# Optimization experiments

Measured on AMD Instinct MI355X. Metric: run time of the kernel, lower is better.

The kernel has to match this reference:

```python
import jax, jax.numpy as jnp
import numpy as np

# Static module config (matches init_kwargs; note forward requires P == Np)
Np = 60   # particles
P  = 60   # per-particle features
Nv = 14   # secondary vertices
S  = 5    # per-vertex features
De = 20
Do = 24
HID = 60
NPP = Np * (Np - 1)
NPV = Np * Nv

# Edge list replacing the dense one-hot Rr/Rs matmuls.
# Edges are all ordered pairs (i, j), i != j, ordered by receiver i then sender j,
# so edges with the same receiver are contiguous (enables reshape+sum scatter).
_pairs = np.array([(i, j) for i in range(Np) for j in range(Np) if i != j], dtype=np.int64)
RECV = jnp.asarray(_pairs[:, 0])  # [NPP]
SEND = jnp.asarray(_pairs[:, 1])  # [NPP]


def _mlp(h, W1, b1, W2, b2):
    return jax.nn.relu(h @ W1 + b1) @ W2 + b2


def setup_inputs() -> dict:
    key = jax.random.key(0)
    ks = jax.random.split(key, 9)
    B = 1024

    def lin(k, fi, fo):
        kw, kb = jax.random.split(k)
        s = 1.0 / np.sqrt(fi)
        W = jax.random.uniform(kw, (fi, fo), minval=-s, maxval=s, dtype=jnp.float32)
        b = jax.random.uniform(kb, (fo,), minval=-s, maxval=s, dtype=jnp.float32)
        return W, b

    W1_pp, b1_pp = lin(ks[0], 2 * P, HID)
    W2_pp, b2_pp = lin(ks[1], HID, De)
    W1_pv, b1_pv = lin(ks[2], P + S, HID)
    W2_pv, b2_pv = lin(ks[3], HID, De)
    W1_o, b1_o = lin(ks[4], P + De, HID)
    W2_o, b2_o = lin(ks[5], HID, Do)
    Wc, bc = lin(ks[6], Do, 1)
    x = jax.random.normal(ks[7], (B, P, Np), dtype=jnp.float32)
    y = jax.random.normal(ks[8], (B, S, Nv), dtype=jnp.float32)
    return dict(x=x, y=y,
                W1_pp=W1_pp, b1_pp=b1_pp, W2_pp=W2_pp, b2_pp=b2_pp,
                W1_pv=W1_pv, b1_pv=b1_pv, W2_pv=W2_pv, b2_pv=b2_pv,
                W1_o=W1_o, b1_o=b1_o, W2_o=W2_o, b2_o=b2_o,
                Wc=Wc, bc=bc)


def reference(x, y, W1_pp, b1_pp, W2_pp, b2_pp, W1_pv, b1_pv, W2_pv, b2_pv,
              W1_o, b1_o, W2_o, b2_o, Wc, bc):
    Bb = x.shape[0]
    # particle-particle branch: gather (x @ Rr, x @ Rs) as index takes
    Orr = jnp.take(x, RECV, axis=2)                  # [B, P, NPP]
    Ors = jnp.take(x, SEND, axis=2)                  # [B, P, NPP]
    Bcat = jnp.concatenate([Orr, Ors], axis=1)       # [B, 2P, NPP]
    # Faithful to the original: B.view(-1, 2P) WITHOUT transposing (row-major flatten)
    E = _mlp(Bcat.reshape(-1, 2 * P), W1_pp, b1_pp, W2_pp, b2_pp).reshape(Bb, NPP, De)
    E = jnp.swapaxes(E, 1, 2)                        # [B, De, NPP]
    # scatter-sum E @ Rr.T : edges grouped by receiver -> reshape+sum
    Ebar_pp = E.reshape(Bb, De, Np, Np - 1).sum(axis=-1)   # [B, De, Np]
    # particle-vertex branch: t = i*Nv + v
    Ork = jnp.repeat(x, Nv, axis=2)                  # [B, P, NPV]  (x @ Rk)
    Orv = jnp.tile(y, (1, 1, Np))                    # [B, S, NPV]  (y @ Rv)
    C = jnp.swapaxes(jnp.concatenate([Ork, Orv], axis=1), 1, 2)  # [B, NPV, P+S]
    F = _mlp(C.reshape(-1, P + S), W1_pv, b1_pv, W2_pv, b2_pv).reshape(Bb, NPV, De)
    F = jnp.swapaxes(F, 1, 2)                        # [B, De, NPV]
    Ebar_pv = F.reshape(Bb, De, Np, Nv).sum(axis=-1)  # F @ Rk.T  -> [B, De, Np]
    Ebar = jnp.swapaxes(Ebar_pp + Ebar_pv, 1, 2)     # [B, Np, De]
    J = jnp.concatenate([x, Ebar], axis=2)           # [B, Np, P+De] (requires P==Np)
    O = _mlp(J.reshape(-1, P + De), W1_o, b1_o, W2_o, b2_o).reshape(Bb, Np, Do)
    O = O.sum(axis=1)                                # transpose+sum over particles -> [B, Do]
    O = O @ Wc + bc                                  # [B, 1]
    return jax.nn.sigmoid(O)
```

## Files before the change

kernel.cpp:

```cpp
#include <hip/hip_runtime.h>
#include <hip/hip_bf16.h>
#include <math.h>

typedef __attribute__((ext_vector_type(8))) short short8;
typedef __attribute__((ext_vector_type(4))) float f32x4;

namespace {
constexpr int XP = 61;
constexpr int EB0 = 3660;
constexpr int Y0 = 4860;
constexpr int ZSLOT = 4930;
constexpr int ARENA_W = 4931;

constexpr int NTAB_PP = 222 * 4 * 64 * 8;
constexpr int NTAB_PV = 53 * 3 * 64 * 8;
constexpr int NTAB_O  = 4 * 3 * 64 * 8;
constexpr int TABPP_B = 0;
constexpr int TABPV_B = TABPP_B + NTAB_PP * 2;
constexpr int TABO_B  = TABPV_B + NTAB_PV * 2;
constexpr int WPP1_B  = TABO_B + NTAB_O * 2;
constexpr int WPP2_B  = WPP1_B + 16 * 64 * 16;
constexpr int WPV1_B  = WPP2_B + 4 * 64 * 16;
constexpr int WPV2_B  = WPV1_B + 12 * 64 * 16;
constexpr int WO1_B   = WPV2_B + 4 * 64 * 16;
constexpr int WO2_B   = WO1_B + 12 * 64 * 16;
constexpr int BIAS_B  = WO2_B + 4 * 64 * 16;
}

__device__ __forceinline__ short f2bfs(float f) {
  __hip_bfloat16 h = __float2bfloat16(f);
  short s;
  __builtin_memcpy(&s, &h, 2);
  return s;
}

__global__ __launch_bounds__(256) void build_tables(char* wsb) {
  int t = blockIdx.x * 256 + threadIdx.x;
  unsigned short* tpp = (unsigned short*)(wsb + TABPP_B);
  unsigned short* tpv = (unsigned short*)(wsb + TABPV_B);
  unsigned short* tou = (unsigned short*)(wsb + TABO_B);
  if (t < NTAB_PP) {
    int j = t & 7, l = (t >> 3) & 63, blk = t >> 9;
    int ks = blk & 3, mt = blk >> 2;
    int rr = mt * 16 + (l & 15), k = ks * 32 + (l >> 4) * 8 + j;
    unsigned off = ZSLOT;
    if (rr < 3540 && k < 120) {
      unsigned p = (unsigned)rr * 120u + (unsigned)k;
      unsigned f = p / 3540u, e = p - f * 3540u;
      unsigned i = e / 59u, jj = e - i * 59u;
      unsigned col = (f < 60u) ? i : ((jj < i) ? jj : jj + 1u);
      unsigned ft = (f < 60u) ? f : f - 60u;
      off = ft * (unsigned)XP + col;
    }
    tpp[t] = (unsigned short)(off * 4u);
    return;
  }
  t -= NTAB_PP;
  if (t < NTAB_PV) {
    int j = t & 7, l = (t >> 3) & 63, blk = t >> 9;
    int ks = blk % 3, mt = blk / 3;
    int tt = mt * 16 + (l & 15), k = ks * 32 + (l >> 4) * 8 + j;
    unsigned off = ZSLOT;
    if (tt < 840 && k < 65) {
      int i = tt / 14, v = tt - i * 14;
      off = (k < 60) ? (unsigned)(k * XP + i) : (unsigned)(Y0 + (k - 60) * 14 + v);
    }
    tpv[t] = (unsigned short)(off * 4u);
    return;
  }
  t -= NTAB_PV;
  if (t < NTAB_O) {
    int j = t & 7, l = (t >> 3) & 63, blk = t >> 9;
    int ks = blk % 3, mt = blk / 3;
    int r = mt * 16 + (l & 15), k = ks * 32 + (l >> 4) * 8 + j;
    unsigned off = ZSLOT;
    if (r < 60 && k < 80)
      off = (k < 60) ? (unsigned)(r * XP + k) : (unsigned)(EB0 + r * 20 + (k - 60));
    tou[t] = (unsigned short)(off * 4u);
  }
}

__global__ __launch_bounds__(256) void build_wfrag(char* wsb,
    const float* W1pp, const float* W2pp, const float* W1pv, const float* W2pv,
    const float* W1o, const float* W2o,
    const float* b1pp, const float* b2pp, const float* b1pv, const float* b2pv,
    const float* b1o, const float* b2o) {
  int t = blockIdx.x * 256 + threadIdx.x;
  if (t < 13312) {
    const float* W; int Kt, Nt, NTt; unsigned* dst; int local;
    if (t < 4096)       { W = W1pp; Kt = 120; Nt = 60; NTt = 4; dst = (unsigned*)(wsb + WPP1_B); local = t; }
    else if (t < 5120)  { W = W2pp; Kt = 60;  Nt = 20; NTt = 2; dst = (unsigned*)(wsb + WPP2_B); local = t - 4096; }
    else if (t < 8192)  { W = W1pv; Kt = 65;  Nt = 60; NTt = 4; dst = (unsigned*)(wsb + WPV1_B); local = t - 5120; }
    else if (t < 9216)  { W = W2pv; Kt = 60;  Nt = 20; NTt = 2; dst = (unsigned*)(wsb + WPV2_B); local = t - 8192; }
    else if (t < 12288) { W = W1o;  Kt = 80;  Nt = 60; NTt = 4; dst = (unsigned*)(wsb + WO1_B);  local = t - 9216; }
    else                { W = W2o;  Kt = 60;  Nt = 24; NTt = 2; dst = (unsigned*)(wsb + WO2_B);  local = t - 12288; }
    int d = local & 3, l = (local >> 2) & 63, rest = local >> 8;
    int nt = rest % NTt, ks = rest / NTt;
    int k = ks * 32 + (l >> 4) * 8 + 2 * d, n = nt * 16 + (l & 15);
    float v0 = (k < Kt && n < Nt) ? W[k * Nt + n] : 0.f;
    float v1 = (k + 1 < Kt && n < Nt) ? W[(k + 1) * Nt + n] : 0.f;
    unsigned u0 = (unsigned short)f2bfs(v0);
    unsigned u1 = (unsigned short)f2bfs(v1);
    dst[local] = u0 | (u1 << 16);
    return;
  }
  t -= 13312;
  if (t < 288) {
    float* bd = (float*)(wsb + BIAS_B);
    float v = 0.f;
    if (t < 64)       { if (t < 60) v = b1pp[t]; }
    else if (t < 96)  { int n = t - 64;  if (n < 20) v = b2pp[n]; }
    else if (t < 160) { int n = t - 96;  if (n < 60) v = b1pv[n]; }
    else if (t < 192) { int n = t - 160; if (n < 20) v = b2pv[n]; }
    else if (t < 256) { int n = t - 192; if (n < 60) v = b1o[n]; }
    else              { int n = t - 256; if (n < 24) v = b2o[n]; }
    bd[t] = v;
  }
}

__device__ __forceinline__ short8 gather8(const char* xb, uint4 tw) {
  float g0 = *(const float*)(xb + (tw.x & 0xffffu));
  float g1 = *(const float*)(xb + (tw.x >> 16));
  float g2 = *(const float*)(xb + (tw.y & 0xffffu));
  float g3 = *(const float*)(xb + (tw.y >> 16));
  float g4 = *(const float*)(xb + (tw.z & 0xffffu));
  float g5 = *(const float*)(xb + (tw.z >> 16));
  float g6 = *(const float*)(xb + (tw.w & 0xffffu));
  float g7 = *(const float*)(xb + (tw.w >> 16));
  short8 af;
  af[0] = f2bfs(g0); af[1] = f2bfs(g1); af[2] = f2bfs(g2); af[3] = f2bfs(g3);
  af[4] = f2bfs(g4); af[5] = f2bfs(g5); af[6] = f2bfs(g6); af[7] = f2bfs(g7);
  return af;
}

template <int NKS>
__device__ __forceinline__ void mlp_tile(
    int mt, int lane, const uint4* __restrict__ tab,
    const short8* wf1, const short8* wf2,
    const float (&b1v)[4], const float (&b2v)[2],
    const float* arena, short (*hrow)[72], f32x4 (&a2)[2])
{
  const int cl = lane & 15, qq = lane >> 4;
  const char* xb = (const char*)arena;

  f32x4 acc[4];
#pragma unroll
  for (int nt = 0; nt < 4; ++nt) {
    float bv = b1v[nt];
    acc[nt] = (f32x4){bv, bv, bv, bv};
  }

#pragma unroll
  for (int ks = 0; ks < NKS; ++ks) {
    uint4 tw = tab[(mt * NKS + ks) * 64 + lane];
    short8 af = gather8(xb, tw);
#pragma unroll
    for (int nt = 0; nt < 4; ++nt) {
      short8 wf = wf1[(ks * 4 + nt) * 64 + lane];
      acc[nt] = __builtin_amdgcn_mfma_f32_16x16x32_bf16(af, wf, acc[nt], 0, 0, 0);
    }
  }

#pragma unroll
  for (int nt = 0; nt < 4; ++nt)
#pragma unroll
    for (int r = 0; r < 4; ++r)
      hrow[qq * 4 + r][nt * 16 + cl] = f2bfs(fmaxf(acc[nt][r], 0.f));

#pragma unroll
  for (int nt = 0; nt < 2; ++nt) {
    float bv = b2v[nt];
    a2[nt] = (f32x4){bv, bv, bv, bv};
  }
#pragma unroll
  for (int k2 = 0; k2 < 2; ++k2) {
    short8 h = *(const short8*)&hrow[cl][k2 * 32 + qq * 8];
#pragma unroll
    for (int nt = 0; nt < 2; ++nt) {
      short8 wf = wf2[(k2 * 2 + nt) * 64 + lane];
      a2[nt] = __builtin_amdgcn_mfma_f32_16x16x32_bf16(h, wf, a2[nt], 0, 0, 0);
    }
  }
}

template <int DIV, int LIM>
__device__ __forceinline__ void scatter_e(const f32x4 (&a2)[2], int rb, float* eb, int cl) {
  int riA = rb / DIV, riB = (rb + 3) / DIV;
#pragma unroll
  for (int nt = 0; nt < 2; ++nt) {
    int col = nt * 16 + cl;
    if (col < 20) {
      if (riA == riB && rb + 3 < LIM) {
        atomicAdd(&eb[riA * 20 + col], a2[nt][0] + a2[nt][1] + a2[nt][2] + a2[nt][3]);
      } else {
#pragma unroll
        for (int r = 0; r < 4; ++r) {
          int rr = rb + r;
          if (rr < LIM) atomicAdd(&eb[(rr / DIV) * 20 + col], a2[nt][r]);
        }
      }
    }
  }
}

__global__ __launch_bounds__(256, 3) void fused_kernel(
    const float* __restrict__ x, const float* __restrict__ y,
    const float* __restrict__ Wc, const float* __restrict__ Bc,
    const char* __restrict__ wsb, float* __restrict__ out) {
  __shared__ float arena[ARENA_W];
  __shared__ __align__(16) short wlds[20 * 64 * 8];
  __shared__ short hlds[4][16][72];
  __shared__ float osum[24];

  const int b = blockIdx.x;
  const int tid = threadIdx.x;
  const int w = tid >> 6;
  const int lane = tid & 63;
  const int cl = lane & 15, q4 = (lane >> 4) * 4;

  for (int k = tid; k < 3600; k += 256) {
    int r = k / 60, c = k - r * 60;
    arena[r * XP + c] = x[(size_t)b * 3600 + k];
  }
  if (tid < 70) arena[Y0 + tid] = y[(size_t)b * 70 + tid];
  for (int k = tid; k < 1200; k += 256) arena[EB0 + k] = 0.f;
  if (tid == 0) arena[ZSLOT] = 0.f;
  if (tid < 24) osum[tid] = 0.f;
  {
    uint4* d = (uint4*)wlds;
    const uint4* sgl = (const uint4*)(wsb + WPP1_B);
    for (int k = tid; k < 1280; k += 256) d[k] = sgl[k];
  }
  __syncthreads();

  const float* biasf = (const float*)(wsb + BIAS_B);

  {
    const short8* wf1 = (const short8*)wlds;
    const short8* wf2 = (const short8*)wlds + 16 * 64;
    const uint4* tab = (const uint4*)(wsb + TABPP_B);
    float b1v[4], b2v[2];
#pragma unroll
    for (int nt = 0; nt < 4; ++nt) b1v[nt] = biasf[0 + nt * 16 + cl];
#pragma unroll
    for (int nt = 0; nt < 2; ++nt) b2v[nt] = biasf[64 + nt * 16 + cl];

    for (int mt = w; mt < 222; mt += 4) {
      f32x4 a2[2];
      mlp_tile<4>(mt, lane, tab, wf1, wf2, b1v, b2v, arena, hlds[w], a2);
      scatter_e<59, 3540>(a2, mt * 16 + q4, &arena[EB0], cl);
    }
  }

  __syncthreads();
  {
    uint4* d = (uint4*)wlds;
    const uint4* sgl = (const uint4*)(wsb + WPV1_B);
    for (int k = tid; k < 1024; k += 256) d[k] = sgl[k];
  }
  __syncthreads();

  {
    const short8* wf1 = (const short8*)wlds;
    const short8* wf2 = (const short8*)wlds + 12 * 64;
    const uint4* tab = (const uint4*)(wsb + TABPV_B);
    float b1v[4], b2v[2];
#pragma unroll
    for (int nt = 0; nt < 4; ++nt) b1v[nt] = biasf[96 + nt * 16 + cl];
#pragma unroll
    for (int nt = 0; nt < 2; ++nt) b2v[nt] = biasf[160 + nt * 16 + cl];

    for (int mt = w; mt < 53; mt += 4) {
      f32x4 a2[2];
      mlp_tile<3>(mt, lane, tab, wf1, wf2, b1v, b2v, arena, hlds[w], a2);
      scatter_e<14, 840>(a2, mt * 16 + q4, &arena[EB0], cl);
    }
  }

  __syncthreads();
  {
    uint4* d = (uint4*)wlds;
    const uint4* sgl = (const uint4*)(wsb + WO1_B);
    for (int k = tid; k < 1024; k += 256) d[k] = sgl[k];
  }
  __syncthreads();

  {
    const short8* wf1 = (const short8*)wlds;
    const short8* wf2 = (const short8*)wlds + 12 * 64;
    const uint4* tab = (const uint4*)(wsb + TABO_B);
    float b1v[4], b2v[2];
#pragma unroll
    for (int nt = 0; nt < 4; ++nt) b1v[nt] = biasf[192 + nt * 16 + cl];
#pragma unroll
    for (int nt = 0; nt < 2; ++nt) b2v[nt] = biasf[256 + nt * 16 + cl];

    f32x4 a2[2];
    mlp_tile<3>(w, lane, tab, wf1, wf2, b1v, b2v, arena, hlds[w], a2);
    int rb = w * 16 + q4;
#pragma unroll
    for (int nt = 0; nt < 2; ++nt) {
      int col = nt * 16 + cl;
      if (col < 24) {
        if (rb + 3 < 60) {
          atomicAdd(&osum[col], a2[nt][0] + a2[nt][1] + a2[nt][2] + a2[nt][3]);
        } else {
#pragma unroll
          for (int r = 0; r < 4; ++r)
            if (rb + r < 60) atomicAdd(&osum[col], a2[nt][r]);
        }
      }
    }
  }

  __syncthreads();
  if (tid == 0) {
    float sd = Bc[0];
#pragma unroll
    for (int o = 0; o < 24; ++o) sd = fmaf(osum[o], Wc[o], sd);
    out[b] = 1.f / (1.f + expf(-sd));
  }
}

extern "C" void kernel_launch(void* const* d_in, const int* in_sizes, int n_in,
                              void* d_out, int out_size, void* d_ws, size_t ws_size,
                              hipStream_t stream) {
  const float* x     = (const float*)d_in[0];
  const float* y     = (const float*)d_in[1];
  const float* W1_pp = (const float*)d_in[2];
  const float* b1_pp = (const float*)d_in[3];
  const float* W2_pp = (const float*)d_in[4];
  const float* b2_pp = (const float*)d_in[5];
  const float* W1_pv = (const float*)d_in[6];
  const float* b1_pv = (const float*)d_in[7];
  const float* W2_pv = (const float*)d_in[8];
  const float* b2_pv = (const float*)d_in[9];
  const float* W1_o  = (const float*)d_in[10];
  const float* b1_o  = (const float*)d_in[11];
  const float* W2_o  = (const float*)d_in[12];
  const float* b2_o  = (const float*)d_in[13];
  const float* Wc    = (const float*)d_in[14];
  const float* bc    = (const float*)d_in[15];
  float* out = (float*)d_out;
  char* wsb = (char*)d_ws;

  const int Bb = in_sizes[0] / 3600;
  const int tab_total = NTAB_PP + NTAB_PV + NTAB_O;

  build_tables<<<(tab_total + 255) / 256, 256, 0, stream>>>(wsb);
  build_wfrag<<<(13600 + 255) / 256, 256, 0, stream>>>(wsb,
      W1_pp, W2_pp, W1_pv, W2_pv, W1_o, W2_o,
      b1_pp, b2_pp, b1_pv, b2_pv, b1_o, b2_o);
  fused_kernel<<<Bb, 256, 0, stream>>>(x, y, Wc, bc, wsb, out);
}
```

Measured before the change: 336.8 us.

## Switch MLP tiles to 32x32x16 MFMA and store activations as bf16 in LDS

Replaces the 16x16x32 bf16 MFMA tiling with 32x32x16 tiles, so each wave handles 32 edge rows per tile with two N-tiles for the hidden layer and one for the output layer. The gather tables, weight fragments and edge-aggregation scatter are re-laid-out to match. The per-block x/y arena and the aggregated edge features are converted to bf16 once at load time, so each gather is a 16-bit LDS read with no per-element conversion. The aim is fewer MFMA issues, fewer table and weight loads, and less conversion work. In exchange the padding waste changes, the output stage uses only two waves, and accumulator register pressure per wave rises.

```diff
diff --git a/kernel.cpp b/kernel.cpp
--- a/kernel.cpp
+++ b/kernel.cpp
@@ -3,34 +3,42 @@
 #include <math.h>
 
 typedef __attribute__((ext_vector_type(8))) short short8;
-typedef __attribute__((ext_vector_type(4))) float f32x4;
+typedef __attribute__((ext_vector_type(16))) float f32x16;
 
 namespace {
-constexpr int XP = 61;
-constexpr int EB0 = 3660;
-constexpr int Y0 = 4860;
-constexpr int ZSLOT = 4930;
-constexpr int ARENA_W = 4931;
-
-constexpr int NTAB_PP = 222 * 4 * 64 * 8;
-constexpr int NTAB_PV = 53 * 3 * 64 * 8;
-constexpr int NTAB_O  = 4 * 3 * 64 * 8;
+constexpr int XB0 = 0;
+constexpr int EBF0 = 7440;
+constexpr int EBB0 = 12240;
+constexpr int YB0 = 14640;
+constexpr int ZS = 14780;
+constexpr int ARENA_B = 14784;
+
+constexpr int NTAB_PP = 111 * 8 * 64 * 8;
+constexpr int NTAB_PV = 27 * 5 * 64 * 8;
+constexpr int NTAB_O  = 2 * 5 * 64 * 8;
 constexpr int TABPP_B = 0;
 constexpr int TABPV_B = TABPP_B + NTAB_PP * 2;
 constexpr int TABO_B  = TABPV_B + NTAB_PV * 2;
 constexpr int WPP1_B  = TABO_B + NTAB_O * 2;
-constexpr int WPP2_B  = WPP1_B + 16 * 64 * 16;
-constexpr int WPV1_B  = WPP2_B + 4 * 64 * 16;
-constexpr int WPV2_B  = WPV1_B + 12 * 64 * 16;
-constexpr int WO1_B   = WPV2_B + 4 * 64 * 16;
-constexpr int WO2_B   = WO1_B + 12 * 64 * 16;
-constexpr int BIAS_B  = WO2_B + 4 * 64 * 16;
+constexpr int WPP2_B  = WPP1_B + 16 * 1024;
+constexpr int WPV1_B  = WPP2_B + 4 * 1024;
+constexpr int WPV2_B  = WPV1_B + 10 * 1024;
+constexpr int WO1_B   = WPV2_B + 4 * 1024;
+constexpr int WO2_B   = WO1_B + 10 * 1024;
+constexpr int BIAS_B  = WO2_B + 4 * 1024;
 }
 
 __device__ __forceinline__ short f2bfs(float f) {
   __hip_bfloat16 h = __float2bfloat16(f);
   short s;
   __builtin_memcpy(&s, &h, 2);
+  return s;
+}
+
+__device__ __forceinline__ f32x16 splat16(float v) {
+  f32x16 s;
+#pragma unroll
+  for (int i = 0; i < 16; ++i) s[i] = v;
   return s;
 }
 
@@ -41,42 +49,44 @@
   unsigned short* tou = (unsigned short*)(wsb + TABO_B);
   if (t < NTAB_PP) {
     int j = t & 7, l = (t >> 3) & 63, blk = t >> 9;
-    int ks = blk & 3, mt = blk >> 2;
-    int rr = mt * 16 + (l & 15), k = ks * 32 + (l >> 4) * 8 + j;
-    unsigned off = ZSLOT;
+    int ks = blk & 7, mt = blk >> 3;
+    int rr = mt * 32 + (l & 31), k = ks * 16 + ((l >> 5) * 8) + j;
+    unsigned off = ZS;
     if (rr < 3540 && k < 120) {
       unsigned p = (unsigned)rr * 120u + (unsigned)k;
       unsigned f = p / 3540u, e = p - f * 3540u;
       unsigned i = e / 59u, jj = e - i * 59u;
       unsigned col = (f < 60u) ? i : ((jj < i) ? jj : jj + 1u);
       unsigned ft = (f < 60u) ? f : f - 60u;
-      off = ft * (unsigned)XP + col;
-    }
-    tpp[t] = (unsigned short)(off * 4u);
+      off = XB0 + (ft * 62u + col) * 2u;
+    }
+    tpp[t] = (unsigned short)off;
     return;
   }
   t -= NTAB_PP;
   if (t < NTAB_PV) {
     int j = t & 7, l = (t >> 3) & 63, blk = t >> 9;
-    int ks = blk % 3, mt = blk / 3;
-    int tt = mt * 16 + (l & 15), k = ks * 32 + (l >> 4) * 8 + j;
-    unsigned off = ZSLOT;
+    int ks = blk % 5, mt = blk / 5;
+    int tt = mt * 32 + (l & 31), k = ks * 16 + ((l >> 5) * 8) + j;
+    unsigned off = ZS;
     if (tt < 840 && k < 65) {
       int i = tt / 14, v = tt - i * 14;
-      off = (k < 60) ? (unsigned)(k * XP + i) : (unsigned)(Y0 + (k - 60) * 14 + v);
-    }
-    tpv[t] = (unsigned short)(off * 4u);
+      off = (k < 60) ? (unsigned)(XB0 + (k * 62 + i) * 2)
+                     : (unsigned)(YB0 + ((k - 60) * 14 + v) * 2);
+    }
+    tpv[t] = (unsigned short)off;
     return;
   }
   t -= NTAB_PV;
   if (t < NTAB_O) {
     int j = t & 7, l = (t >> 3) & 63, blk = t >> 9;
-    int ks = blk % 3, mt = blk / 3;
-    int r = mt * 16 + (l & 15), k = ks * 32 + (l >> 4) * 8 + j;
-    unsigned off = ZSLOT;
+    int ks = blk % 5, mt = blk / 5;
+    int r = mt * 32 + (l & 31), k = ks * 16 + ((l >> 5) * 8) + j;
+    unsigned off = ZS;
     if (r < 60 && k < 80)
-      off = (k < 60) ? (unsigned)(r * XP + k) : (unsigned)(EB0 + r * 20 + (k - 60));
-    tou[t] = (unsigned short)(off * 4u);
+      off = (k < 60) ? (unsigned)(XB0 + (r * 62 + k) * 2)
+                     : (unsigned)(EBB0 + (r * 20 + (k - 60)) * 2);
+    tou[t] = (unsigned short)off;
   }
 }
 
@@ -86,17 +96,17 @@
     const float* b1pp, const float* b2pp, const float* b1pv, const float* b2pv,
     const float* b1o, const float* b2o) {
   int t = blockIdx.x * 256 + threadIdx.x;
-  if (t < 13312) {
-    const float* W; int Kt, Nt, NTt; unsigned* dst; int local;
-    if (t < 4096)       { W = W1pp; Kt = 120; Nt = 60; NTt = 4; dst = (unsigned*)(wsb + WPP1_B); local = t; }
-    else if (t < 5120)  { W = W2pp; Kt = 60;  Nt = 20; NTt = 2; dst = (unsigned*)(wsb + WPP2_B); local = t - 4096; }
-    else if (t < 8192)  { W = W1pv; Kt = 65;  Nt = 60; NTt = 4; dst = (unsigned*)(wsb + WPV1_B); local = t - 5120; }
-    else if (t < 9216)  { W = W2pv; Kt = 60;  Nt = 20; NTt = 2; dst = (unsigned*)(wsb + WPV2_B); local = t - 8192; }
-    else if (t < 12288) { W = W1o;  Kt = 80;  Nt = 60; NTt = 4; dst = (unsigned*)(wsb + WO1_B);  local = t - 9216; }
-    else                { W = W2o;  Kt = 60;  Nt = 24; NTt = 2; dst = (unsigned*)(wsb + WO2_B);  local = t - 12288; }
-    int d = local & 3, l = (local >> 2) & 63, rest = local >> 8;
-    int nt = rest % NTt, ks = rest / NTt;
-    int k = ks * 32 + (l >> 4) * 8 + 2 * d, n = nt * 16 + (l & 15);
+  if (t < 12288) {
+    const float* W; int Kt, Nt, NT; unsigned* dst; int local;
+    if (t < 4096)        { W = W1pp; Kt = 120; Nt = 60; NT = 2; dst = (unsigned*)(wsb + WPP1_B); local = t; }
+    else if (t < 5120)   { W = W2pp; Kt = 60;  Nt = 20; NT = 1; dst = (unsigned*)(wsb + WPP2_B); local = t - 4096; }
+    else if (t < 7680)   { W = W1pv; Kt = 65;  Nt = 60; NT = 2; dst = (unsigned*)(wsb + WPV1_B); local = t - 5120; }
+    else if (t < 8704)   { W = W2pv; Kt = 60;  Nt = 20; NT = 1; dst = (unsigned*)(wsb + WPV2_B); local = t - 7680; }
+    else if (t < 11264)  { W = W1o;  Kt = 80;  Nt = 60; NT = 2; dst = (unsigned*)(wsb + WO1_B);  local = t - 8704; }
+    else                 { W = W2o;  Kt = 60;  Nt = 24; NT = 1; dst = (unsigned*)(wsb + WO2_B);  local = t - 11264; }
+    int d = local & 3, l = (local >> 2) & 63, fi = local >> 8;
+    int nt = fi % NT, ks = fi / NT;
+    int k = ks * 16 + (l >> 5) * 8 + 2 * d, n = nt * 32 + (l & 31);
     float v0 = (k < Kt && n < Nt) ? W[k * Nt + n] : 0.f;
     float v1 = (k + 1 < Kt && n < Nt) ? W[(k + 1) * Nt + n] : 0.f;
     unsigned u0 = (unsigned short)f2bfs(v0);
@@ -104,7 +114,7 @@
     dst[local] = u0 | (u1 << 16);
     return;
   }
-  t -= 13312;
+  t -= 12288;
   if (t < 288) {
     float* bd = (float*)(wsb + BIAS_B);
     float v = 0.f;
@@ -118,85 +128,70 @@
   }
 }
 
-__device__ __forceinline__ short8 gather8(const char* xb, uint4 tw) {
-  float g0 = *(const float*)(xb + (tw.x & 0xffffu));
-  float g1 = *(const float*)(xb + (tw.x >> 16));
-  float g2 = *(const float*)(xb + (tw.y & 0xffffu));
-  float g3 = *(const float*)(xb + (tw.y >> 16));
-  float g4 = *(const float*)(xb + (tw.z & 0xffffu));
-  float g5 = *(const float*)(xb + (tw.z >> 16));
-  float g6 = *(const float*)(xb + (tw.w & 0xffffu));
-  float g7 = *(const float*)(xb + (tw.w >> 16));
-  short8 af;
-  af[0] = f2bfs(g0); af[1] = f2bfs(g1); af[2] = f2bfs(g2); af[3] = f2bfs(g3);
-  af[4] = f2bfs(g4); af[5] = f2bfs(g5); af[6] = f2bfs(g6); af[7] = f2bfs(g7);
-  return af;
-}
-
 template <int NKS>
-__device__ __forceinline__ void mlp_tile(
+__device__ __forceinline__ void mlp32(
     int mt, int lane, const uint4* __restrict__ tab,
     const short8* wf1, const short8* wf2,
-    const float (&b1v)[4], const float (&b2v)[2],
-    const float* arena, short (*hrow)[72], f32x4 (&a2)[2])
+    float b1a, float b1b, float b2,
+    const unsigned char* arena_b, short (*hrow)[72], f32x16& eo)
 {
-  const int cl = lane & 15, qq = lane >> 4;
-  const char* xb = (const char*)arena;
-
-  f32x4 acc[4];
-#pragma unroll
-  for (int nt = 0; nt < 4; ++nt) {
-    float bv = b1v[nt];
-    acc[nt] = (f32x4){bv, bv, bv, bv};
-  }
+  const int cl = lane & 31, hi = lane >> 5;
+
+  f32x16 acc0 = splat16(b1a);
+  f32x16 acc1 = splat16(b1b);
 
 #pragma unroll
   for (int ks = 0; ks < NKS; ++ks) {
     uint4 tw = tab[(mt * NKS + ks) * 64 + lane];
-    short8 af = gather8(xb, tw);
-#pragma unroll
-    for (int nt = 0; nt < 4; ++nt) {
-      short8 wf = wf1[(ks * 4 + nt) * 64 + lane];
-      acc[nt] = __builtin_amdgcn_mfma_f32_16x16x32_bf16(af, wf, acc[nt], 0, 0, 0);
-    }
-  }
-
-#pragma unroll
-  for (int nt = 0; nt < 4; ++nt)
-#pragma unroll
-    for (int r = 0; r < 4; ++r)
-      hrow[qq * 4 + r][nt * 16 + cl] = f2bfs(fmaxf(acc[nt][r], 0.f));
-
-#pragma unroll
-  for (int nt = 0; nt < 2; ++nt) {
-    float bv = b2v[nt];
-    a2[nt] = (f32x4){bv, bv, bv, bv};
-  }
-#pragma unroll
-  for (int k2 = 0; k2 < 2; ++k2) {
-    short8 h = *(const short8*)&hrow[cl][k2 * 32 + qq * 8];
-#pragma unroll
-    for (int nt = 0; nt < 2; ++nt) {
-      short8 wf = wf2[(k2 * 2 + nt) * 64 + lane];
-      a2[nt] = __builtin_amdgcn_mfma_f32_16x16x32_bf16(h, wf, a2[nt], 0, 0, 0);
-    }
-  }
+    short8 af;
+    af[0] = *(const short*)(arena_b + (tw.x & 0xffffu));
+    af[1] = *(const short*)(arena_b + (tw.x >> 16));
+    af[2] = *(const short*)(arena_b + (tw.y & 0xffffu));
+    af[3] = *(const short*)(arena_b + (tw.y >> 16));
+    af[4] = *(const short*)(arena_b + (tw.z & 0xffffu));
+    af[5] = *(const short*)(arena_b + (tw.z >> 16));
+    af[6] = *(const short*)(arena_b + (tw.w & 0xffffu));
+    af[7] = *(const short*)(arena_b + (tw.w >> 16));
+    short8 w0 = wf1[(ks * 2 + 0) * 64 + lane];
+    short8 w1 = wf1[(ks * 2 + 1) * 64 + lane];
+    acc0 = __builtin_amdgcn_mfma_f32_32x32x16_bf16(af, w0, acc0, 0, 0, 0);
+    acc1 = __builtin_amdgcn_mfma_f32_32x32x16_bf16(af, w1, acc1, 0, 0, 0);
+  }
+
+#pragma unroll
+  for (int g = 0; g < 4; ++g)
+#pragma unroll
+    for (int q = 0; q < 4; ++q) {
+      int row = q + 8 * g + 4 * hi;
+      int reg = g * 4 + q;
+      hrow[row][cl] = f2bfs(fmaxf(acc0[reg], 0.f));
+      hrow[row][32 + cl] = f2bfs(fmaxf(acc1[reg], 0.f));
+    }
+
+  f32x16 a2 = splat16(b2);
+#pragma unroll
+  for (int ks2 = 0; ks2 < 4; ++ks2) {
+    short8 h = *(const short8*)&hrow[cl][ks2 * 16 + hi * 8];
+    short8 w = wf2[ks2 * 64 + lane];
+    a2 = __builtin_amdgcn_mfma_f32_32x32x16_bf16(h, w, a2, 0, 0, 0);
+  }
+  eo = a2;
 }
 
 template <int DIV, int LIM>
-__device__ __forceinline__ void scatter_e(const f32x4 (&a2)[2], int rb, float* eb, int cl) {
-  int riA = rb / DIV, riB = (rb + 3) / DIV;
-#pragma unroll
-  for (int nt = 0; nt < 2; ++nt) {
-    int col = nt * 16 + cl;
-    if (col < 20) {
-      if (riA == riB && rb + 3 < LIM) {
-        atomicAdd(&eb[riA * 20 + col], a2[nt][0] + a2[nt][1] + a2[nt][2] + a2[nt][3]);
+__device__ __forceinline__ void scatter32(const f32x16& e, int rb, float* eb, int cl, int hi) {
+  if (cl < 20) {
+#pragma unroll
+    for (int g = 0; g < 4; ++g) {
+      int r0 = rb + 8 * g + 4 * hi;
+      if (r0 / DIV == (r0 + 3) / DIV && r0 + 3 < LIM) {
+        atomicAdd(&eb[(r0 / DIV) * 20 + cl],
+                  e[4 * g] + e[4 * g + 1] + e[4 * g + 2] + e[4 * g + 3]);
       } else {
 #pragma unroll
-        for (int r = 0; r < 4; ++r) {
-          int rr = rb + r;
-          if (rr < LIM) atomicAdd(&eb[(rr / DIV) * 20 + col], a2[nt][r]);
+        for (int q = 0; q < 4; ++q) {
+          int rr = r0 + q;
+          if (rr < LIM) atomicAdd(&eb[(rr / DIV) * 20 + cl], e[4 * g + q]);
         }
       }
     }
@@ -207,107 +202,98 @@
     const float* __restrict__ x, const float* __restrict__ y,
     const float* __restrict__ Wc, const float* __restrict__ Bc,
     const char* __restrict__ wsb, float* __restrict__ out) {
-  __shared__ float arena[ARENA_W];
-  __shared__ __align__(16) short wlds[20 * 64 * 8];
-  __shared__ short hlds[4][16][72];
+  __shared__ __align__(16) unsigned char arena_b[ARENA_B];
+  __shared__ __align__(16) short wlds[10240];
+  __shared__ __align__(16) short hlds[4][32][72];
   __shared__ float osum[24];
 
   const int b = blockIdx.x;
   const int tid = threadIdx.x;
   const int w = tid >> 6;
   const int lane = tid & 63;
-  const int cl = lane & 15, q4 = (lane >> 4) * 4;
-
-  for (int k = tid; k < 3600; k += 256) {
-    int r = k / 60, c = k - r * 60;
-    arena[r * XP + c] = x[(size_t)b * 3600 + k];
-  }
-  if (tid < 70) arena[Y0 + tid] = y[(size_t)b * 70 + tid];
-  for (int k = tid; k < 1200; k += 256) arena[EB0 + k] = 0.f;
-  if (tid == 0) arena[ZSLOT] = 0.f;
-  if (tid < 24) osum[tid] = 0.f;
-  {
+  const int cl = lane & 31, hi = lane >> 5;
+
+  {
+    short* xb = (short*)(arena_b + XB0);
+    for (int k = tid; k < 3600; k += 256) {
+      int r = k / 60, c = k - r * 60;
+      xb[r * 62 + c] = f2bfs(x[(size_t)b * 3600 + k]);
+    }
+    short* yb = (short*)(arena_b + YB0);
+    if (tid < 70) yb[tid] = f2bfs(y[(size_t)b * 70 + tid]);
+    float* ebf = (float*)(arena_b + EBF0);
+    for (int k = tid; k < 1200; k += 256) ebf[k] = 0.f;
+    if (tid == 0) *(short*)(arena_b + ZS) = 0;
+    if (tid < 24) osum[tid] = 0.f;
     uint4* d = (uint4*)wlds;
-    const uint4* sgl = (const uint4*)(wsb + WPP1_B);
-    for (int k = tid; k < 1280; k += 256) d[k] = sgl[k];
+    const uint4* s = (const uint4*)(wsb + WPP1_B);
+    for (int k = tid; k < 1280; k += 256) d[k] = s[k];
   }
   __syncthreads();
 
   const float* biasf = (const float*)(wsb + BIAS_B);
+  float* ebf = (float*)(arena_b + EBF0);
 
   {
     const short8* wf1 = (const short8*)wlds;
     const short8* wf2 = (const short8*)wlds + 16 * 64;
     const uint4* tab = (const uint4*)(wsb + TABPP_B);
-    float b1v[4], b2v[2];
-#pragma unroll
-    for (int nt = 0; nt < 4; ++nt) b1v[nt] = biasf[0 + nt * 16 + cl];
-#pragma unroll
-    for (int nt = 0; nt < 2; ++nt) b2v[nt] = biasf[64 + nt * 16 + cl];
-
-    for (int mt = w; mt < 222; mt += 4) {
-      f32x4 a2[2];
-      mlp_tile<4>(mt, lane, tab, wf1, wf2, b1v, b2v, arena, hlds[w], a2);
-      scatter_e<59, 3540>(a2, mt * 16 + q4, &arena[EB0], cl);
+    float b1a = biasf[0 + cl], b1b = biasf[32 + cl], b2 = biasf[64 + cl];
+    for (int mt = w; mt < 111; mt += 4) {
+      f32x16 e;
+      mlp32<8>(mt, lane, tab, wf1, wf2, b1a, b1b, b2, arena_b, hlds[w], e);
+      scatter32<59, 3540>(e, mt * 32, ebf, cl, hi);
     }
   }
 
   __syncthreads();
   {
     uint4* d = (uint4*)wlds;
-    const uint4* sgl = (const uint4*)(wsb + WPV1_B);
-    for (int k = tid; k < 1024; k += 256) d[k] = sgl[k];
+    const uint4* s = (const uint4*)(wsb + WPV1_B);
+    for (int k = tid; k < 896; k += 256) d[k] = s[k];
   }
   __syncthreads();
 
   {
     const short8* wf1 = (const short8*)wlds;
-    const short8* wf2 = (const short8*)wlds + 12 * 64;
+    const short8* wf2 = (const short8*)wlds + 10 * 64;
     const uint4* tab = (const uint4*)(wsb + TABPV_B);
-    float b1v[4], b2v[2];
-#pragma unroll
-    for (int nt = 0; nt < 4; ++nt) b1v[nt] = biasf[96 + nt * 16 + cl];
-#pragma unroll
-    for (int nt = 0; nt < 2; ++nt) b2v[nt] = biasf[160 + nt * 16 + cl];
-
-    for (int mt = w; mt < 53; mt += 4) {
-      f32x4 a2[2];
-      mlp_tile<3>(mt, lane, tab, wf1, wf2, b1v, b2v, arena, hlds[w], a2);
-      scatter_e<14, 840>(a2, mt * 16 + q4, &arena[EB0], cl);
-    }
-  }
-
-  __syncthreads();
-  {
+    float b1a = biasf[96 + cl], b1b = biasf[128 + cl], b2 = biasf[160 + cl];
+    for (int mt = w; mt < 27; mt += 4) {
+      f32x16 e;
+      mlp32<5>(mt, lane, tab, wf1, wf2, b1a, b1b, b2, arena_b, hlds[w], e);
+      scatter32<14, 840>(e, mt * 32, ebf, cl, hi);
+    }
+  }
+
+  __syncthreads();
+  {
+    short* ebb = (short*)(arena_b + EBB0);
+    for (int k = tid; k < 1200; k += 256) ebb[k] = f2bfs(ebf[k]);
     uint4* d = (uint4*)wlds;
-    const uint4* sgl = (const uint4*)(wsb + WO1_B);
-    for (int k = tid; k < 1024; k += 256) d[k] = sgl[k];
-  }
-  __syncthreads();
-
-  {
+    const uint4* s = (const uint4*)(wsb + WO1_B);
+    for (int k = tid; k < 896; k += 256) d[k] = s[k];
+  }
+  __syncthreads();
+
+  if (w < 2) {
     const short8* wf1 = (const short8*)wlds;
-    const short8* wf2 = (const short8*)wlds + 12 * 64;
+    const short8* wf2 = (const short8*)wlds + 10 * 64;
     const uint4* tab = (const uint4*)(wsb + TABO_B);
-    float b1v[4], b2v[2];
-#pragma unroll
-    for (int nt = 0; nt < 4; ++nt) b1v[nt] = biasf[192 + nt * 16 + cl];
-#pragma unroll
-    for (int nt = 0; nt < 2; ++nt) b2v[nt] = biasf[256 + nt * 16 + cl];
-
-    f32x4 a2[2];
-    mlp_tile<3>(w, lane, tab, wf1, wf2, b1v, b2v, arena, hlds[w], a2);
-    int rb = w * 16 + q4;
-#pragma unroll
-    for (int nt = 0; nt < 2; ++nt) {
-      int col = nt * 16 + cl;
-      if (col < 24) {
-        if (rb + 3 < 60) {
-          atomicAdd(&osum[col], a2[nt][0] + a2[nt][1] + a2[nt][2] + a2[nt][3]);
+    float b1a = biasf[192 + cl], b1b = biasf[224 + cl], b2 = biasf[256 + cl];
+    f32x16 e;
+    mlp32<5>(w, lane, tab, wf1, wf2, b1a, b1b, b2, arena_b, hlds[w], e);
+    int rb = w * 32;
+    if (cl < 24) {
+#pragma unroll
+      for (int g = 0; g < 4; ++g) {
+        int r0 = rb + 8 * g + 4 * hi;
+        if (r0 + 3 < 60) {
+          atomicAdd(&osum[cl], e[4 * g] + e[4 * g + 1] + e[4 * g + 2] + e[4 * g + 3]);
         } else {
 #pragma unroll
-          for (int r = 0; r < 4; ++r)
-            if (rb + r < 60) atomicAdd(&osum[col], a2[nt][r]);
+          for (int q = 0; q < 4; ++q)
+            if (r0 + q < 60) atomicAdd(&osum[cl], e[4 * g + q]);
         }
       }
     }
@@ -348,7 +334,7 @@
   const int tab_total = NTAB_PP + NTAB_PV + NTAB_O;
 
   build_tables<<<(tab_total + 255) / 256, 256, 0, stream>>>(wsb);
-  build_wfrag<<<(13600 + 255) / 256, 256, 0, stream>>>(wsb,
+  build_wfrag<<<(12288 + 288 + 255) / 256, 256, 0, stream>>>(wsb,
       W1_pp, W2_pp, W1_pv, W2_pv, W1_o, W2_o,
       b1_pp, b2_pp, b1_pv, b2_pv, b1_o, b2_o);
   fused_kernel<<<Bb, 256, 0, stream>>>(x, y, Wc, bc, wsb, out);
```

After: 382.0 us. 1.13x slower.

## Stage inputs as bf16 in LDS, prefetch gather tables, keep W2 in registers

Applied to the files above, without the earlier changes.

Converts x, y and the aggregated edge sums to bf16 once when staging them into shared memory, so the MFMA gather reads 2-byte values without per-element conversion. Gather-offset tables are software-prefetched one tile ahead, and second-layer weight fragments are held in registers instead of LDS. The shared arena is repacked into one byte buffer small enough to raise launch bounds to 4 blocks per SM. Register pressure from the prefetch and weight registers may constrain occupancy, and Ebar is now rounded to bf16 before the output MLP.

```diff
diff --git a/kernel.cpp b/kernel.cpp
--- a/kernel.cpp
+++ b/kernel.cpp
@@ -6,11 +6,15 @@
 typedef __attribute__((ext_vector_type(4))) float f32x4;
 
 namespace {
-constexpr int XP = 61;
-constexpr int EB0 = 3660;
-constexpr int Y0 = 4860;
-constexpr int ZSLOT = 4930;
-constexpr int ARENA_W = 4931;
+constexpr int XB0    = 0;
+constexpr int YB0    = 7440;
+constexpr int ZSB    = 7580;
+constexpr int EBF_B  = 7584;
+constexpr int WLDS_B = 12384;
+constexpr int EBB_B  = 24672;
+constexpr int HLDS_B = 28768;
+constexpr int OSUM_B = 37984;
+constexpr int SM_BYTES = 38080;
 
 constexpr int NTAB_PP = 222 * 4 * 64 * 8;
 constexpr int NTAB_PV = 53 * 3 * 64 * 8;
@@ -19,12 +23,12 @@
 constexpr int TABPV_B = TABPP_B + NTAB_PP * 2;
 constexpr int TABO_B  = TABPV_B + NTAB_PV * 2;
 constexpr int WPP1_B  = TABO_B + NTAB_O * 2;
-constexpr int WPP2_B  = WPP1_B + 16 * 64 * 16;
-constexpr int WPV1_B  = WPP2_B + 4 * 64 * 16;
-constexpr int WPV2_B  = WPV1_B + 12 * 64 * 16;
-constexpr int WO1_B   = WPV2_B + 4 * 64 * 16;
-constexpr int WO2_B   = WO1_B + 12 * 64 * 16;
-constexpr int BIAS_B  = WO2_B + 4 * 64 * 16;
+constexpr int WPP2_B  = WPP1_B + 16 * 1024;
+constexpr int WPV1_B  = WPP2_B + 4 * 1024;
+constexpr int WPV2_B  = WPV1_B + 12 * 1024;
+constexpr int WO1_B   = WPV2_B + 4 * 1024;
+constexpr int WO2_B   = WO1_B + 12 * 1024;
+constexpr int BIAS_B  = WO2_B + 4 * 1024;
 }
 
 __device__ __forceinline__ short f2bfs(float f) {
@@ -43,16 +47,16 @@
     int j = t & 7, l = (t >> 3) & 63, blk = t >> 9;
     int ks = blk & 3, mt = blk >> 2;
     int rr = mt * 16 + (l & 15), k = ks * 32 + (l >> 4) * 8 + j;
-    unsigned off = ZSLOT;
+    unsigned off = ZSB;
     if (rr < 3540 && k < 120) {
       unsigned p = (unsigned)rr * 120u + (unsigned)k;
       unsigned f = p / 3540u, e = p - f * 3540u;
       unsigned i = e / 59u, jj = e - i * 59u;
       unsigned col = (f < 60u) ? i : ((jj < i) ? jj : jj + 1u);
       unsigned ft = (f < 60u) ? f : f - 60u;
-      off = ft * (unsigned)XP + col;
-    }
-    tpp[t] = (unsigned short)(off * 4u);
+      off = XB0 + (ft * 62u + col) * 2u;
+    }
+    tpp[t] = (unsigned short)off;
     return;
   }
   t -= NTAB_PP;
@@ -60,12 +64,13 @@
     int j = t & 7, l = (t >> 3) & 63, blk = t >> 9;
     int ks = blk % 3, mt = blk / 3;
     int tt = mt * 16 + (l & 15), k = ks * 32 + (l >> 4) * 8 + j;
-    unsigned off = ZSLOT;
+    unsigned off = ZSB;
     if (tt < 840 && k < 65) {
       int i = tt / 14, v = tt - i * 14;
-      off = (k < 60) ? (unsigned)(k * XP + i) : (unsigned)(Y0 + (k - 60) * 14 + v);
-    }
-    tpv[t] = (unsigned short)(off * 4u);
+      off = (k < 60) ? (unsigned)(XB0 + (k * 62 + i) * 2)
+                     : (unsigned)(YB0 + ((k - 60) * 14 + v) * 2);
+    }
+    tpv[t] = (unsigned short)off;
     return;
   }
   t -= NTAB_PV;
@@ -73,10 +78,11 @@
     int j = t & 7, l = (t >> 3) & 63, blk = t >> 9;
     int ks = blk % 3, mt = blk / 3;
     int r = mt * 16 + (l & 15), k = ks * 32 + (l >> 4) * 8 + j;
-    unsigned off = ZSLOT;
+    unsigned off = ZSB;
     if (r < 60 && k < 80)
-      off = (k < 60) ? (unsigned)(r * XP + k) : (unsigned)(EB0 + r * 20 + (k - 60));
-    tou[t] = (unsigned short)(off * 4u);
+      off = (k < 60) ? (unsigned)(XB0 + (r * 62 + k) * 2)
+                     : (unsigned)(EBB_B + (r * 20 + (k - 60)) * 2);
+    tou[t] = (unsigned short)off;
   }
 }
 
@@ -118,30 +124,15 @@
   }
 }
 
-__device__ __forceinline__ short8 gather8(const char* xb, uint4 tw) {
-  float g0 = *(const float*)(xb + (tw.x & 0xffffu));
-  float g1 = *(const float*)(xb + (tw.x >> 16));
-  float g2 = *(const float*)(xb + (tw.y & 0xffffu));
-  float g3 = *(const float*)(xb + (tw.y >> 16));
-  float g4 = *(const float*)(xb + (tw.z & 0xffffu));
-  float g5 = *(const float*)(xb + (tw.z >> 16));
-  float g6 = *(const float*)(xb + (tw.w & 0xffffu));
-  float g7 = *(const float*)(xb + (tw.w >> 16));
-  short8 af;
-  af[0] = f2bfs(g0); af[1] = f2bfs(g1); af[2] = f2bfs(g2); af[3] = f2bfs(g3);
-  af[4] = f2bfs(g4); af[5] = f2bfs(g5); af[6] = f2bfs(g6); af[7] = f2bfs(g7);
-  return af;
-}
-
 template <int NKS>
-__device__ __forceinline__ void mlp_tile(
-    int mt, int lane, const uint4* __restrict__ tab,
-    const short8* wf1, const short8* wf2,
+__device__ __forceinline__ void mlp_core(
+    const uint4 (&tw)[NKS], int lane,
+    const short8* wf1,
+    const short8 (&wf2r)[4],
     const float (&b1v)[4], const float (&b2v)[2],
-    const float* arena, short (*hrow)[72], f32x4 (&a2)[2])
+    const unsigned char* smb, short (*hrow)[72], f32x4 (&a2)[2])
 {
   const int cl = lane & 15, qq = lane >> 4;
-  const char* xb = (const char*)arena;
 
   f32x4 acc[4];
 #pragma unroll
@@ -152,8 +143,15 @@
 
 #pragma unroll
   for (int ks = 0; ks < NKS; ++ks) {
-    uint4 tw = tab[(mt * NKS + ks) * 64 + lane];
-    short8 af = gather8(xb, tw);
+    short8 af;
+    af[0] = *(const short*)(smb + (tw[ks].x & 0xffffu));
+    af[1] = *(const short*)(smb + (tw[ks].x >> 16));
+    af[2] = *(const short*)(smb + (tw[ks].y & 0xffffu));
+    af[3] = *(const short*)(smb + (tw[ks].y >> 16));
+    af[4] = *(const short*)(smb + (tw[ks].z & 0xffffu));
+    af[5] = *(const short*)(smb + (tw[ks].z >> 16));
+    af[6] = *(const short*)(smb + (tw[ks].w & 0xffffu));
+    af[7] = *(const short*)(smb + (tw[ks].w >> 16));
 #pragma unroll
     for (int nt = 0; nt < 4; ++nt) {
       short8 wf = wf1[(ks * 4 + nt) * 64 + lane];
@@ -176,10 +174,8 @@
   for (int k2 = 0; k2 < 2; ++k2) {
     short8 h = *(const short8*)&hrow[cl][k2 * 32 + qq * 8];
 #pragma unroll
-    for (int nt = 0; nt < 2; ++nt) {
-      short8 wf = wf2[(k2 * 2 + nt) * 64 + lane];
-      a2[nt] = __builtin_amdgcn_mfma_f32_16x16x32_bf16(h, wf, a2[nt], 0, 0, 0);
-    }
+    for (int nt = 0; nt < 2; ++nt)
+      a2[nt] = __builtin_amdgcn_mfma_f32_16x16x32_bf16(h, wf2r[k2 * 2 + nt], a2[nt], 0, 0, 0);
   }
 }
 
@@ -203,14 +199,11 @@
   }
 }
 
-__global__ __launch_bounds__(256, 3) void fused_kernel(
+__global__ __launch_bounds__(256, 4) void fused_kernel(
     const float* __restrict__ x, const float* __restrict__ y,
     const float* __restrict__ Wc, const float* __restrict__ Bc,
     const char* __restrict__ wsb, float* __restrict__ out) {
-  __shared__ float arena[ARENA_W];
-  __shared__ __align__(16) short wlds[20 * 64 * 8];
-  __shared__ short hlds[4][16][72];
-  __shared__ float osum[24];
+  __shared__ __align__(16) unsigned char SM[SM_BYTES];
 
   const int b = blockIdx.x;
   const int tid = threadIdx.x;
@@ -218,85 +211,126 @@
   const int lane = tid & 63;
   const int cl = lane & 15, q4 = (lane >> 4) * 4;
 
-  for (int k = tid; k < 3600; k += 256) {
-    int r = k / 60, c = k - r * 60;
-    arena[r * XP + c] = x[(size_t)b * 3600 + k];
-  }
-  if (tid < 70) arena[Y0 + tid] = y[(size_t)b * 70 + tid];
-  for (int k = tid; k < 1200; k += 256) arena[EB0 + k] = 0.f;
-  if (tid == 0) arena[ZSLOT] = 0.f;
-  if (tid < 24) osum[tid] = 0.f;
-  {
-    uint4* d = (uint4*)wlds;
-    const uint4* sgl = (const uint4*)(wsb + WPP1_B);
-    for (int k = tid; k < 1280; k += 256) d[k] = sgl[k];
-  }
-  __syncthreads();
-
+  float* ebf = (float*)(SM + EBF_B);
+  float* osum = (float*)(SM + OSUM_B);
+  short (*hrow)[72] = (short(*)[72])(SM + HLDS_B + w * 2304);
   const float* biasf = (const float*)(wsb + BIAS_B);
 
   {
-    const short8* wf1 = (const short8*)wlds;
-    const short8* wf2 = (const short8*)wlds + 16 * 64;
+    short* xb = (short*)(SM + XB0);
+    for (int k = tid; k < 3600; k += 256) {
+      int r = k / 60, c = k - r * 60;
+      xb[r * 62 + c] = f2bfs(x[(size_t)b * 3600 + k]);
+    }
+    short* yb = (short*)(SM + YB0);
+    if (tid < 70) yb[tid] = f2bfs(y[(size_t)b * 70 + tid]);
+    if (tid == 0) *(short*)(SM + ZSB) = 0;
+    for (int k = tid; k < 1200; k += 256) ebf[k] = 0.f;
+    if (tid < 24) osum[tid] = 0.f;
+    uint4* d = (uint4*)(SM + WLDS_B);
+    const uint4* s = (const uint4*)(wsb + WPP1_B);
+    for (int k = tid; k < 1024; k += 256) d[k] = s[k];
+  }
+  __syncthreads();
+
+  {
+    const short8* wf1 = (const short8*)(SM + WLDS_B);
     const uint4* tab = (const uint4*)(wsb + TABPP_B);
+    short8 wf2r[4];
+#pragma unroll
+    for (int i = 0; i < 4; ++i) wf2r[i] = ((const short8*)(wsb + WPP2_B))[i * 64 + lane];
     float b1v[4], b2v[2];
 #pragma unroll
     for (int nt = 0; nt < 4; ++nt) b1v[nt] = biasf[0 + nt * 16 + cl];
 #pragma unroll
     for (int nt = 0; nt < 2; ++nt) b2v[nt] = biasf[64 + nt * 16 + cl];
 
+    uint4 twn[4];
+#pragma unroll
+    for (int ks = 0; ks < 4; ++ks) twn[ks] = tab[(w * 4 + ks) * 64 + lane];
     for (int mt = w; mt < 222; mt += 4) {
+      uint4 twc[4];
+#pragma unroll
+      for (int ks = 0; ks < 4; ++ks) twc[ks] = twn[ks];
+      int mtn = mt + 4;
+      if (mtn < 222) {
+#pragma unroll
+        for (int ks = 0; ks < 4; ++ks) twn[ks] = tab[(mtn * 4 + ks) * 64 + lane];
+      }
       f32x4 a2[2];
-      mlp_tile<4>(mt, lane, tab, wf1, wf2, b1v, b2v, arena, hlds[w], a2);
-      scatter_e<59, 3540>(a2, mt * 16 + q4, &arena[EB0], cl);
-    }
-  }
-
-  __syncthreads();
-  {
-    uint4* d = (uint4*)wlds;
-    const uint4* sgl = (const uint4*)(wsb + WPV1_B);
-    for (int k = tid; k < 1024; k += 256) d[k] = sgl[k];
-  }
-  __syncthreads();
-
-  {
-    const short8* wf1 = (const short8*)wlds;
-    const short8* wf2 = (const short8*)wlds + 12 * 64;
+      mlp_core<4>(twc, lane, wf1, wf2r, b1v, b2v, SM, hrow, a2);
+      scatter_e<59, 3540>(a2, mt * 16 + q4, ebf, cl);
+    }
+  }
+
+  __syncthreads();
+  {
+    uint4* d = (uint4*)(SM + WLDS_B);
+    const uint4* s = (const uint4*)(wsb + WPV1_B);
+    for (int k = tid; k < 768; k += 256) d[k] = s[k];
+  }
+  __syncthreads();
+
+  {
+    const short8* wf1 = (const short8*)(SM + WLDS_B);
     const uint4* tab = (const uint4*)(wsb + TABPV_B);
+    short8 wf2r[4];
+#pragma unroll
+    for (int i = 0; i < 4; ++i) wf2r[i] = ((const short8*)(wsb + WPV2_B))[i * 64 + lane];
     float b1v[4], b2v[2];
 #pragma unroll
     for (int nt = 0; nt < 4; ++nt) b1v[nt] = biasf[96 + nt * 16 + cl];
 #pragma unroll
     for (int nt = 0; nt < 2; ++nt) b2v[nt] = biasf[160 + nt * 16 + cl];
 
+    uint4 twn[3];
+    if (w < 53) {
+#pragma unroll
+      for (int ks = 0; ks < 3; ++ks) twn[ks] = tab[(w * 3 + ks) * 64 + lane];
+    }
     for (int mt = w; mt < 53; mt += 4) {
+      uint4 twc[3];
+#pragma unroll
+      for (int ks = 0; ks < 3; ++ks) twc[ks] = twn[ks];
+      int mtn = mt + 4;
+      if (mtn < 53) {
+#pragma unroll
+        for (int ks = 0; ks < 3; ++ks) twn[ks] = tab[(mtn * 3 + ks) * 64 + lane];
+      }
       f32x4 a2[2];
-      mlp_tile<3>(mt, lane, tab, wf1, wf2, b1v, b2v, arena, hlds[w], a2);
-      scatter_e<14, 840>(a2, mt * 16 + q4, &arena[EB0], cl);
-    }
-  }
-
-  __syncthreads();
-  {
-    uint4* d = (uint4*)wlds;
-    const uint4* sgl = (const uint4*)(wsb + WO1_B);
-    for (int k = tid; k < 1024; k += 256) d[k] = sgl[k];
-  }
-  __syncthreads();
-
-  {
-    const short8* wf1 = (const short8*)wlds;
-    const short8* wf2 = (const short8*)wlds + 12 * 64;
+      mlp_core<3>(twc, lane, wf1, wf2r, b1v, b2v, SM, hrow, a2);
+      scatter_e<14, 840>(a2, mt * 16 + q4, ebf, cl);
+    }
+  }
+
+  __syncthreads();
+  {
+    short* ebb = (short*)(SM + EBB_B);
+    for (int k = tid; k < 1200; k += 256) ebb[k] = f2bfs(ebf[k]);
+    uint4* d = (uint4*)(SM + WLDS_B);
+    const uint4* s = (const uint4*)(wsb + WO1_B);
+    for (int k = tid; k < 768; k += 256) d[k] = s[k];
+  }
+  __syncthreads();
+
+  {
+    const short8* wf1 = (const short8*)(SM + WLDS_B);
     const uint4* tab = (const uint4*)(wsb + TABO_B);
+    short8 wf2r[4];
+#pragma unroll
+    for (int i = 0; i < 4; ++i) wf2r[i] = ((const short8*)(wsb + WO2_B))[i * 64 + lane];
     float b1v[4], b2v[2];
 #pragma unroll
     for (int nt = 0; nt < 4; ++nt) b1v[nt] = biasf[192 + nt * 16 + cl];
 #pragma unroll
     for (int nt = 0; nt < 2; ++nt) b2v[nt] = biasf[256 + nt * 16 + cl];
 
+    uint4 twc[3];
+#pragma unroll
+    for (int ks = 0; ks < 3; ++ks) twc[ks] = tab[(w * 3 + ks) * 64 + lane];
     f32x4 a2[2];
-    mlp_tile<3>(w, lane, tab, wf1, wf2, b1v, b2v, arena, hlds[w], a2);
+    mlp_core<3>(twc, lane, wf1, wf2r, b1v, b2v, SM, hrow, a2);
+
     int rb = w * 16 + q4;
 #pragma unroll
     for (int nt = 0; nt < 2; ++nt) {
@@ -348,7 +382,7 @@
   const int tab_total = NTAB_PP + NTAB_PV + NTAB_O;
 
   build_tables<<<(tab_total + 255) / 256, 256, 0, stream>>>(wsb);
-  build_wfrag<<<(13600 + 255) / 256, 256, 0, stream>>>(wsb,
+  build_wfrag<<<(13312 + 288 + 255) / 256, 256, 0, stream>>>(wsb,
       W1_pp, W2_pp, W1_pv, W2_pv, W1_o, W2_o,
       b1_pp, b2_pp, b1_pv, b2_pv, b1_o, b2_o);
   fused_kernel<<<Bb, 256, 0, stream>>>(x, y, Wc, bc, wsb, out);
```

After: 353.9 us. 5.1% more time.
